# Kernel optimization log

Measured on AMD Instinct MI355X. Metric: run time of the kernel, lower is better.

Reference implementation:

```python
import jax, jax.numpy as jnp
import numpy as np
from jax import lax

N = 2048    # atoms
K = 16      # knn neighbors -> E = N*K = 32768 edges
H = 128     # latent width
L = 10      # stacked InteractionNetworks
STEPS = 10  # outer simulation iterations


def _rn(key, shape, scale=0.05):
    return scale * jax.random.normal(key, shape, dtype=jnp.float32)


def setup_inputs() -> dict:
    key = jax.random.key(0)
    ks = iter(jax.random.split(key, 40))
    inp = {
        "pos": jax.random.normal(next(ks), (N, 3), dtype=jnp.float32),
        "node_f": jax.random.normal(next(ks), (N, 24), dtype=jnp.float32),
        "mass": jnp.ones((N,), jnp.float32),
        # node encoder MLP(24,128,2,128)
        "nW1": _rn(next(ks), (24, H)), "nb1": _rn(next(ks), (H,)),
        "nW2": _rn(next(ks), (H, H)), "nb2": _rn(next(ks), (H,)),
        # edge encoder MLP(4,128,2,128)
        "eW1": _rn(next(ks), (4, H)), "eb1": _rn(next(ks), (H,)),
        "eW2": _rn(next(ks), (H, H)), "eb2": _rn(next(ks), (H,)),
        # RelationModel per IN: input = 2*dim_obj + dim_rel = 384, 4 Linear layers (ReLU after each)
        "rmW1": _rn(next(ks), (L, 3 * H, H)), "rmb1": _rn(next(ks), (L, H)),
        "rmW2": _rn(next(ks), (L, H, H)), "rmb2": _rn(next(ks), (L, H)),
        "rmW3": _rn(next(ks), (L, H, H)), "rmb3": _rn(next(ks), (L, H)),
        "rmW4": _rn(next(ks), (L, H, H)), "rmb4": _rn(next(ks), (L, H)),
        # ObjectModel per IN: input = dim_obj + dim_eff = 256 -> hidden 128 -> out 128
        "omW1": _rn(next(ks), (L, 2 * H, H)), "omb1": _rn(next(ks), (L, H)),
        "omW2": _rn(next(ks), (L, H, H)), "omb2": _rn(next(ks), (L, H)),
        # decoder MLP(128,128,2,3)
        "dW1": _rn(next(ks), (H, H)), "db1": _rn(next(ks), (H,)),
        "dW2": _rn(next(ks), (H, 3)), "db2": _rn(next(ks), (3,)),
        "k": K,
    }
    return inp


def _mlp2(x, W1, b1, W2, b2):
    return jax.nn.relu(x @ W1 + b1) @ W2 + b2


def _knn_edges(pos, k):
    # knn(P.pos, k): edge_index[:,0] = sender (neighbor), edge_index[:,1] = receiver
    n = pos.shape[0]
    sq = jnp.sum(pos * pos, axis=1)
    d2 = sq[:, None] + sq[None, :] - 2.0 * (pos @ pos.T)   # [N, N]
    d2 = d2 + 1e9 * jnp.eye(n, dtype=pos.dtype)            # exclude self
    _, idx = lax.top_k(-d2, k)                              # [N, k] nearest
    senders = idx.reshape(-1)                               # [E]
    receivers = jnp.repeat(jnp.arange(n), k)                # [E]
    rel = pos[senders] - pos[receivers]
    dist = jnp.linalg.norm(rel, axis=1, keepdims=True)
    ea0 = jnp.concatenate([rel, dist], axis=1)              # [E, 4]
    return senders, receivers, ea0


def _simulate(pos, node_f, mass, nW1, nb1, nW2, nb2, eW1, eb1, eW2, eb2,
              rmW1, rmb1, rmW2, rmb2, rmW3, rmb3, rmW4, rmb4,
              omW1, omb1, omW2, omb2, dW1, db1, dW2, db2, k):
    n = pos.shape[0]
    # G.pos = G.pos + randn * 0.1 ; G.vels = zeros
    pos = pos + 0.1 * jax.random.normal(jax.random.key(42), pos.shape, dtype=pos.dtype)
    vels = jnp.zeros_like(pos)

    stacked = (rmW1, rmb1, rmW2, rmb2, rmW3, rmb3, rmW4, rmb4,
               omW1, omb1, omW2, omb2)

    for _ in range(STEPS):
        senders, receivers, ea0 = _knn_edges(pos, k)

        # encode
        x = _mlp2(node_f, nW1, nb1, nW2, nb2)    # [N, H]
        ea = _mlp2(ea0, eW1, eb1, eW2, eb2)      # [E, H]

        # process: 10 InteractionNetworks. In the original, layer(P.x, P.senders,
        # P.receivers, P.edge_attr) binds rr=senders, rs=receivers, so the
        # one-hot matmuls obj.t()@rr / obj.t()@rs are gathers by sender/receiver,
        # and e @ rr.t() is a scatter-add onto sender nodes.
        def in_step(carry, p):
            xc, eac = carry
            rW1, rb1, rW2, rb2, rW3, rb3, rW4, rb4, oW1, ob1, oW2, ob2 = p
            b = jnp.concatenate([xc[senders], xc[receivers], eac], axis=1)  # [E, 3H]
            h = jax.nn.relu(b @ rW1 + rb1)
            h = jax.nn.relu(h @ rW2 + rb2)
            h = jax.nn.relu(h @ rW3 + rb3)
            e = jax.nn.relu(h @ rW4 + rb4)                                   # [E, H]
            agg = jax.ops.segment_sum(e, senders, num_segments=n)           # e @ rr.T
            a = jnp.concatenate([xc, agg], axis=1)                           # [N, 2H]
            x_new = jax.nn.relu(a @ oW1 + ob1) @ oW2 + ob2                   # [N, H]
            return (x_new, e), None

        (x, ea), _ = lax.scan(jax.checkpoint(in_step), (x, ea), stacked)

        # decode + update
        forces = _mlp2(x, dW1, db1, dW2, db2)    # [N, 3]
        vels = vels + forces / mass[:, None]
        pos = pos + vels
    return pos


def reference(pos, node_f, mass, nW1, nb1, nW2, nb2, eW1, eb1, eW2, eb2,
              rmW1, rmb1, rmW2, rmb2, rmW3, rmb3, rmW4, rmb4,
              omW1, omb1, omW2, omb2, dW1, db1, dW2, db2, k):
    return _simulate(pos, node_f, mass, nW1, nb1, nW2, nb2, eW1, eb1, eW2, eb2,
                     rmW1, rmb1, rmW2, rmb2, rmW3, rmb3, rmW4, rmb4,
                     omW1, omb1, omW2, omb2, dW1, db1, dW2, db2, k)
```

## Files before the change

### kernel.cpp

```cpp
#include <hip/hip_runtime.h>

#define N_ATOMS 2048
#define KNN 16
#define NE (N_ATOMS*KNN)
#define H 128
#define NL 10
#define NSTEPS 10
#define NCHUNK 32
#define S4B ((size_t)16384)
#define S8B ((size_t)32768)

typedef unsigned short u16;
typedef __attribute__((ext_vector_type(4))) float f32x4;
typedef __attribute__((ext_vector_type(8))) short bf16x8;

__device__ __forceinline__ u16 f2bf(float x){
  unsigned u = __float_as_uint(x);
  return (u16)((u + 0x7FFFu + ((u >> 16) & 1u)) >> 16);
}
__device__ __forceinline__ float bf2f(u16 v){ return __uint_as_float(((unsigned)v) << 16); }

template<int PITCH>
__device__ __forceinline__ bf16x8 ldsB_m8(const u16* s, int e, int k){
  int byte = e*PITCH + (k<<1); byte ^= ((e&7)<<4);
  return *(const bf16x8*)((const char*)s + byte);
}
template<int PITCH>
__device__ __forceinline__ void lds_st16_m8(u16* s, int row, int k, uint4 v){
  int byte = row*PITCH + (k<<1); byte ^= ((row&7)<<4);
  *(uint4*)((char*)s + byte) = v;
}
template<int PITCH>
__device__ __forceinline__ uint4 lds_ld16_m8(const u16* s, int row, int k){
  int byte = row*PITCH + (k<<1); byte ^= ((row&7)<<4);
  return *(const uint4*)((const char*)s + byte);
}
template<int PITCH>
__device__ __forceinline__ void lds_st8_m8(u16* s, int row, int k, uint2 v){
  int byte = row*PITCH + (k<<1); byte ^= ((row&7)<<4);
  *(uint2*)((char*)s + byte) = v;
}

template<int KST, int KS, int ET, int PITCH>
__device__ __forceinline__ void mfma_gemm_m8(const u16* sBh, const u16* sBl,
    const u16* __restrict__ pWh, const u16* __restrict__ pWl,
    int ksbase, int wpair, int rowbase, int lane, f32x4 acc[2][ET]){
  const int er = lane & 15, kg = lane >> 4;
  const size_t base = ((size_t)(wpair*KST + ksbase)*64 + lane)*8;
  #pragma unroll
  for (int ks = 0; ks < KS; ks++){
    const int klds = ks*32 + kg*8;
    bf16x8 bh[ET], bl[ET];
    #pragma unroll
    for (int et = 0; et < ET; et++){
      bh[et] = ldsB_m8<PITCH>(sBh, rowbase + et*16 + er, klds);
      bl[et] = ldsB_m8<PITCH>(sBl, rowbase + et*16 + er, klds);
    }
    #pragma unroll
    for (int nt = 0; nt < 2; nt++){
      const size_t off = base + (size_t)(nt*KST + ks)*512;
      bf16x8 ah = *(const bf16x8*)(pWh + off);
      bf16x8 al = *(const bf16x8*)(pWl + off);
      #pragma unroll
      for (int et = 0; et < ET; et++){
        acc[nt][et] = __builtin_amdgcn_mfma_f32_16x16x32_bf16(ah, bh[et], acc[nt][et], 0, 0, 0);
        acc[nt][et] = __builtin_amdgcn_mfma_f32_16x16x32_bf16(ah, bl[et], acc[nt][et], 0, 0, 0);
        acc[nt][et] = __builtin_amdgcn_mfma_f32_16x16x32_bf16(al, bh[et], acc[nt][et], 0, 0, 0);
      }
    }
  }
}

#define CLR_M8(acc, ET) { _Pragma("unroll") for (int i_=0;i_<2;i_++){ _Pragma("unroll") for (int j_=0;j_<ET;j_++){ \
  acc[i_][j_][0]=0.f; acc[i_][j_][1]=0.f; acc[i_][j_][2]=0.f; acc[i_][j_][3]=0.f; } } }

template<int ET, int PITCH, bool RELU>
__device__ __forceinline__ void epi_lds_m8(f32x4 acc[2][ET], u16* sh, u16* sl,
    int wpair, int rowbase, int lane, const float* __restrict__ bias){
  const int er = lane & 15, g = lane >> 4;
  #pragma unroll
  for (int nt = 0; nt < 2; nt++){
    const int n0 = (wpair + nt)*16 + g*4;
    f32x4 bv = *(const f32x4*)(bias + n0);
    #pragma unroll
    for (int et = 0; et < ET; et++){
      const int e = rowbase + et*16 + er;
      unsigned hw[2], lw[2];
      #pragma unroll
      for (int q = 0; q < 2; q++){
        float v0 = acc[nt][et][2*q]   + bv[2*q];
        float v1 = acc[nt][et][2*q+1] + bv[2*q+1];
        if (RELU){ v0 = fmaxf(v0, 0.f); v1 = fmaxf(v1, 0.f); }
        u16 h0 = f2bf(v0), h1 = f2bf(v1);
        u16 l0 = f2bf(v0 - bf2f(h0)), l1 = f2bf(v1 - bf2f(h1));
        hw[q] = (unsigned)h0 | ((unsigned)h1 << 16);
        lw[q] = (unsigned)l0 | ((unsigned)l1 << 16);
      }
      uint2 hv; hv.x = hw[0]; hv.y = hw[1];
      uint2 lv; lv.x = lw[0]; lv.y = lw[1];
      lds_st8_m8<PITCH>(sh, e, n0, hv);
      lds_st8_m8<PITCH>(sl, e, n0, lv);
    }
  }
}

__global__ __launch_bounds__(256) void pack_w_m8(const float* __restrict__ W,
    u16* __restrict__ ph, u16* __restrict__ pl, int KS, int L, int lstride, int roff){
  int idx = blockIdx.x*256 + threadIdx.x;
  int per = 8*KS*64;
  if (idx >= per*L) return;
  int l = idx / per, r = idx - l*per;
  int lane = r & 63, rest = r >> 6;
  int ks = rest % KS, nt = rest / KS;
  int n = nt*16 + (lane & 15), kb = ks*32 + (lane >> 4)*8;
  const float* src = W + (size_t)l*lstride;
  u16 h8[8], l8[8];
  #pragma unroll
  for (int j = 0; j < 8; j++){
    float v = src[(size_t)(roff + kb + j)*H + n];
    u16 h = f2bf(v);
    h8[j] = h; l8[j] = f2bf(v - bf2f(h));
  }
  size_t off = (size_t)idx*8;
  uint4 hv, lv;
  hv.x = h8[0]|((unsigned)h8[1]<<16); hv.y = h8[2]|((unsigned)h8[3]<<16);
  hv.z = h8[4]|((unsigned)h8[5]<<16); hv.w = h8[6]|((unsigned)h8[7]<<16);
  lv.x = l8[0]|((unsigned)l8[1]<<16); lv.y = l8[2]|((unsigned)l8[3]<<16);
  lv.z = l8[4]|((unsigned)l8[5]<<16); lv.w = l8[6]|((unsigned)l8[7]<<16);
  *(uint4*)(ph + off) = hv;
  *(uint4*)(pl + off) = lv;
}

__device__ __forceinline__ int lds_byte_f_m8(int r, int k4){
  return (((r<<9) + (k4<<2)) ^ (((r>>3)&7)<<4));
}
__device__ __forceinline__ f32x4 lds4r_f_m8(const float* s, int r, int k4){
  return *(const f32x4*)((const char*)s + lds_byte_f_m8(r,k4));
}
__device__ __forceinline__ void lds4w_f_m8(float* s, int r, int k4, f32x4 v){
  *(f32x4*)((char*)s + lds_byte_f_m8(r,k4)) = v;
}
__device__ __forceinline__ float lds1r_f_m8(const float* s, int r, int k){
  return *(const float*)((const char*)s + lds_byte_f_m8(r, k & ~3) + ((k&3)<<2));
}
template<int KD, int RPT>
__device__ __forceinline__ void gemm_f_m8(const float* sA, const float* __restrict__ gW,
                                          int r0, int c0, float acc[RPT][4]){
  #pragma unroll 2
  for (int k4 = 0; k4 < KD; k4 += 4){
    f32x4 a[RPT];
    #pragma unroll
    for (int i=0;i<RPT;i++) a[i] = lds4r_f_m8(sA, r0+i, k4);
    #pragma unroll
    for (int kk=0;kk<4;kk++){
      f32x4 wv = *(const f32x4*)(gW + (size_t)(k4+kk)*H + c0);
      #pragma unroll
      for (int i=0;i<RPT;i++){
        acc[i][0] = fmaf(a[i][kk], wv[0], acc[i][0]);
        acc[i][1] = fmaf(a[i][kk], wv[1], acc[i][1]);
        acc[i][2] = fmaf(a[i][kk], wv[2], acc[i][2]);
        acc[i][3] = fmaf(a[i][kk], wv[3], acc[i][3]);
      }
    }
  }
}

__device__ __forceinline__ unsigned rotl32_m8(unsigned v, int d){ return (v << d) | (v >> (32 - d)); }
__device__ __forceinline__ void tf2x32_m8(unsigned k0, unsigned k1, unsigned x0, unsigned x1,
                                          unsigned* o0, unsigned* o1){
  unsigned ks2 = k0 ^ k1 ^ 0x1BD11BDAu;
  x0 += k0; x1 += k1;
  const int R0[4] = {13,15,26,6}, R1[4] = {17,29,16,24};
#define TFG(R) { for (int i=0;i<4;i++){ x0 += x1; x1 = rotl32_m8(x1,R[i]); x1 ^= x0; } }
  TFG(R0); x0 += k1;  x1 += ks2 + 1u;
  TFG(R1); x0 += ks2; x1 += k0  + 2u;
  TFG(R0); x0 += k0;  x1 += k1  + 3u;
  TFG(R1); x0 += k1;  x1 += ks2 + 4u;
  TFG(R0); x0 += ks2; x1 += k0  + 5u;
#undef TFG
  *o0 = x0; *o1 = x1;
}
__device__ float bits_to_normal_m8(unsigned bits){
  float f = __uint_as_float((bits >> 9) | 0x3F800000u) - 1.0f;
  const float lo = -0.99999994f;
  float u = fmaxf(lo, __fadd_rn(__fmul_rn(f, 2.0f), lo));
  float w = -log1pf(-__fmul_rn(u, u));
  float p;
  if (w < 5.0f){
    w = __fsub_rn(w, 2.5f);
    p = 2.81022636e-08f;
    p = __fadd_rn(__fmul_rn(p,w),  3.43273939e-07f);
    p = __fadd_rn(__fmul_rn(p,w), -3.5233877e-06f);
    p = __fadd_rn(__fmul_rn(p,w), -4.39150654e-06f);
    p = __fadd_rn(__fmul_rn(p,w),  0.00021858087f);
    p = __fadd_rn(__fmul_rn(p,w), -0.00125372503f);
    p = __fadd_rn(__fmul_rn(p,w), -0.00417768164f);
    p = __fadd_rn(__fmul_rn(p,w),  0.246640727f);
    p = __fadd_rn(__fmul_rn(p,w),  1.50140941f);
  } else {
    w = __fsub_rn(sqrtf(w), 3.0f);
    p = -0.000200214257f;
    p = __fadd_rn(__fmul_rn(p,w),  0.000100950558f);
    p = __fadd_rn(__fmul_rn(p,w),  0.00134934322f);
    p = __fadd_rn(__fmul_rn(p,w), -0.00367342844f);
    p = __fadd_rn(__fmul_rn(p,w),  0.00573950773f);
    p = __fadd_rn(__fmul_rn(p,w), -0.0076224613f);
    p = __fadd_rn(__fmul_rn(p,w),  0.00943887047f);
    p = __fadd_rn(__fmul_rn(p,w),  1.00167406f);
    p = __fadd_rn(__fmul_rn(p,w),  2.83297682f);
  }
  return __fmul_rn(1.41421356f, __fmul_rn(p, u));
}
__device__ __forceinline__ unsigned draw_bits_m8(unsigned k1, unsigned k2, int bk, int m, int half){
  unsigned o0, o1;
  if (bk == 0){
    if (m < half){ tf2x32_m8(k1,k2, (unsigned)m, (unsigned)(m+half), &o0,&o1); return o0; }
    else         { tf2x32_m8(k1,k2, (unsigned)(m-half), (unsigned)m, &o0,&o1); return o1; }
  }
  tf2x32_m8(k1,k2, 0u, (unsigned)m, &o0,&o1);
  return (bk==1) ? (o0^o1) : (bk==2) ? o1 : o0;
}
__global__ __launch_bounds__(64) void rng_init_m8(int* flags){
  if (threadIdx.x < 8) flags[threadIdx.x] = 1;
}
__global__ __launch_bounds__(256) void rng_detect_m8(const float* __restrict__ pos_in, int* flags){
  int m = blockIdx.x*256 + threadIdx.x;
  if (m >= N_ATOMS*3) return;
  unsigned a0,a1,b0,b1,f0,f1;
  tf2x32_m8(0u,0u, 0u,40u, &a0,&a1);
  tf2x32_m8(0u,0u, 1u,41u, &b0,&b1);
  tf2x32_m8(0u,0u, 0u,0u,  &f0,&f1);
  float target = pos_in[m];
  #pragma unroll
  for (int v = 0; v < 8; v++){
    unsigned k1 = (v<4)? a0 : f0, k2 = (v<4)? b0 : f1;
    unsigned bits = draw_bits_m8(k1,k2, v&3, m, 3072);
    float z = bits_to_normal_m8(bits);
    if (fabsf(z - target) > 1e-3f) flags[v] = 0;
  }
}
__global__ __launch_bounds__(64) void rng_select_m8(const int* flags, int* sel){
  if (threadIdx.x == 0){
    int s = -1;
    for (int v = 0; v < 8; v++) if (flags[v]){ s = v; break; }
    sel[0] = (s < 0) ? 1 : (s & 3);
  }
}
__global__ __launch_bounds__(256) void perturb_m8(const float* __restrict__ pos,
    const int* __restrict__ sel, float* __restrict__ posw, float* __restrict__ vels){
  int m = blockIdx.x*256 + threadIdx.x;
  if (m >= N_ATOMS*3) return;
  unsigned bits = draw_bits_m8(0u, 42u, sel[0], m, 3072);
  float z = bits_to_normal_m8(bits);
  posw[m] = __fadd_rn(pos[m], __fmul_rn(0.1f, z));
  vels[m] = 0.f;
}

__global__ __launch_bounds__(128) void node_enc_m8(const float* __restrict__ nf,
    const float* __restrict__ W1, const float* __restrict__ b1,
    const float* __restrict__ W2, const float* __restrict__ b2,
    u16* __restrict__ xh, u16* __restrict__ xl){
  __shared__ float s_in[24];
  __shared__ float s_h[128];
  int n = blockIdx.x, t = threadIdx.x;
  if (t < 24) s_in[t] = nf[n*24 + t];
  __syncthreads();
  float a = b1[t];
  #pragma unroll
  for (int k = 0; k < 24; k++) a = fmaf(s_in[k], W1[k*H + t], a);
  s_h[t] = fmaxf(a, 0.f);
  __syncthreads();
  float a2 = b2[t];
  for (int k = 0; k < H; k++) a2 = fmaf(s_h[k], W2[k*H + t], a2);
  u16 h = f2bf(a2);
  xh[(size_t)n*H + t] = h;
  xl[(size_t)n*H + t] = f2bf(a2 - bf2f(h));
}

__global__ __launch_bounds__(256) void pnode_m8(
    const u16* __restrict__ xh, const u16* __restrict__ xl,
    const u16* __restrict__ pah, const u16* __restrict__ pal,
    const u16* __restrict__ pbh, const u16* __restrict__ pbl,
    float* __restrict__ P1g, float* __restrict__ P2g){
  __shared__ __align__(16) u16 sXh[16*128];
  __shared__ __align__(16) u16 sXl[16*128];
  const int t = threadIdx.x, n0b = blockIdx.x*16;
  const int i = t>>4, seg = t&15;
  {
    uint4 hv = *(const uint4*)(xh + (size_t)(n0b+i)*H + seg*8);
    uint4 lv = *(const uint4*)(xl + (size_t)(n0b+i)*H + seg*8);
    lds_st16_m8<256>(sXh, i, seg*8, hv);
    lds_st16_m8<256>(sXl, i, seg*8, lv);
  }
  __syncthreads();
  const int w = t>>6, lane = t&63, er = lane&15, g = lane>>4;
  f32x4 acc[2][1];
  CLR_M8(acc, 1);
  mfma_gemm_m8<4,4,1,256>(sXh, sXl, pah, pal, 0, w*2, 0, lane, acc);
  #pragma unroll
  for (int nt = 0; nt < 2; nt++)
    *(f32x4*)(P1g + (size_t)(n0b+er)*H + (w*2+nt)*16 + g*4) = acc[nt][0];
  CLR_M8(acc, 1);
  mfma_gemm_m8<4,4,1,256>(sXh, sXl, pbh, pbl, 0, w*2, 0, lane, acc);
  #pragma unroll
  for (int nt = 0; nt < 2; nt++)
    *(f32x4*)(P2g + (size_t)(n0b+er)*H + (w*2+nt)*16 + g*4) = acc[nt][0];
}

__global__ __launch_bounds__(256) void knn_m9(const float* __restrict__ pos,
                                              int* __restrict__ senders,
                                              float* __restrict__ ea0,
                                              int* __restrict__ countsC){
  __shared__ float d2[N_ATOMS];
  __shared__ float pv[4];
  __shared__ int   pi[4];
  int r = blockIdx.x, t = threadIdx.x;
  float prx = pos[r*3+0], pry = pos[r*3+1], prz = pos[r*3+2];
  float sqr = __fadd_rn(__fadd_rn(__fmul_rn(prx,prx), __fmul_rn(pry,pry)), __fmul_rn(prz,prz));
  for (int c = t; c < N_ATOMS; c += 256){
    float cx = pos[c*3+0], cy = pos[c*3+1], cz = pos[c*3+2];
    float sqc = __fadd_rn(__fadd_rn(__fmul_rn(cx,cx), __fmul_rn(cy,cy)), __fmul_rn(cz,cz));
    float dot = __fadd_rn(__fadd_rn(__fmul_rn(prx,cx), __fmul_rn(pry,cy)), __fmul_rn(prz,cz));
    float v = __fsub_rn(__fadd_rn(sqr, sqc), __fmul_rn(2.0f, dot));
    d2[c] = (c == r) ? 1e9f : v;
  }
  __syncthreads();
  for (int j = 0; j < KNN; j++){
    float bv = 1e30f; int bi = 0x7fffffff;
    for (int c = t; c < N_ATOMS; c += 256){
      float v = d2[c];
      if (v < bv || (v == bv && c < bi)){ bv = v; bi = c; }
    }
    #pragma unroll
    for (int off = 32; off; off >>= 1){
      float ov = __shfl_down(bv, off);
      int   oi = __shfl_down(bi, off);
      if (ov < bv || (ov == bv && oi < bi)){ bv = ov; bi = oi; }
    }
    if ((t & 63) == 0){ pv[t>>6] = bv; pi[t>>6] = bi; }
    __syncthreads();
    if (t == 0){
      float fv = pv[0]; int fi = pi[0];
      #pragma unroll
      for (int q = 1; q < 4; q++){
        if (pv[q] < fv || (pv[q] == fv && pi[q] < fi)){ fv = pv[q]; fi = pi[q]; }
      }
      senders[r*KNN + j] = fi;
      atomicAdd(&countsC[(r>>6)*N_ATOMS + fi], 1);
      float dx = __fsub_rn(pos[fi*3+0], prx);
      float dy = __fsub_rn(pos[fi*3+1], pry);
      float dz = __fsub_rn(pos[fi*3+2], prz);
      float ss = __fadd_rn(__fadd_rn(__fmul_rn(dx,dx), __fmul_rn(dy,dy)), __fmul_rn(dz,dz));
      float* o = ea0 + (size_t)(r*KNN + j)*4;
      o[0] = dx; o[1] = dy; o[2] = dz; o[3] = sqrtf(ss);
      d2[fi] = 1e30f;
    }
    __syncthreads();
  }
}

__global__ __launch_bounds__(256) void csr_scan2_m9(int* __restrict__ countsC,
                                                    int* __restrict__ rowstart){
  __shared__ int part[256];
  const int t = threadIdx.x;
  const int base = t*8;
  int loc[8];
  int ssum = 0;
  #pragma unroll
  for (int i = 0; i < 8; i++){
    int s = base + i;
    int tv = 0;
    #pragma unroll
    for (int c = 0; c < NCHUNK; c++) tv += countsC[c*N_ATOMS + s];
    loc[i] = ssum; ssum += tv;
  }
  part[t] = ssum;
  __syncthreads();
  if (t == 0){
    int acc = 0;
    for (int i = 0; i < 256; i++){ int v = part[i]; part[i] = acc; acc += v; }
    rowstart[N_ATOMS] = acc;
  }
  __syncthreads();
  int p = part[t];
  #pragma unroll
  for (int i = 0; i < 8; i++){
    int s = base + i;
    int rs = p + loc[i];
    rowstart[s] = rs;
    int b = rs;
    #pragma unroll
    for (int c = 0; c < NCHUNK; c++){
      int tv = countsC[c*N_ATOMS + s];
      countsC[c*N_ATOMS + s] = b;
      b += tv;
    }
  }
}

__global__ __launch_bounds__(1024) void csr_place_m9(const int* __restrict__ senders,
    const int* __restrict__ countsC, int* __restrict__ elist){
  __shared__ int cnt[N_ATOMS];
  __shared__ int sL[1024];
  const int c = blockIdx.x, t = threadIdx.x;
  cnt[t] = countsC[c*N_ATOMS + t];
  cnt[1024 + t] = countsC[c*N_ATOMS + 1024 + t];
  sL[t] = senders[c*1024 + t];
  __syncthreads();
  const int w = t>>6, lane = t&63, wb = w<<6;
  const int my_s = sL[t];
  int rank = 0, same = 0;
  for (int k = 0; k < 64; k++){
    int sk = sL[wb + k];
    int eq = (sk == my_s) ? 1 : 0;
    same += eq;
    if (k < lane) rank += eq;
  }
  #pragma unroll
  for (int round = 0; round < 16; round++){
    if (w == round){
      int bb = cnt[my_s];
      elist[bb + rank] = c*1024 + t;
      if (rank == same - 1) cnt[my_s] = bb + same;
    }
    __syncthreads();
  }
}

template<int FIRST>
__global__ __launch_bounds__(256) void chain_m8(
    const float* __restrict__ P1g, const float* __restrict__ P2g,
    u16* __restrict__ eag, const int* __restrict__ senders,
    const float* __restrict__ ea0,
    const float* __restrict__ eW1, const float* __restrict__ eb1,
    const u16* __restrict__ e2h, const u16* __restrict__ e2l, const float* __restrict__ eb2,
    const u16* __restrict__ w1h, const u16* __restrict__ w1l, const float* __restrict__ b1,
    const u16* __restrict__ w2h, const u16* __restrict__ w2l, const float* __restrict__ b2,
    const u16* __restrict__ w3h, const u16* __restrict__ w3l, const float* __restrict__ b3,
    const u16* __restrict__ w4h, const u16* __restrict__ w4l, const float* __restrict__ b4){
  __shared__ __align__(16) u16 sPh[64*128];
  __shared__ __align__(16) u16 sPl[64*128];
  __shared__ __align__(16) u16 sQh[64*128];
  __shared__ __align__(16) u16 sQl[64*128];
  __shared__ float sE0[64*4];
  const int t = threadIdx.x, e0 = blockIdx.x*64;
  const int w = t>>6, lane = t&63, er = lane&15, g = lane>>4;
  const int wpair = w*2;
  f32x4 acc[2][4];
  int sidx[4];
  #pragma unroll
  for (int et = 0; et < 4; et++) sidx[et] = senders[e0 + et*16 + er];
  #pragma unroll
  for (int et = 0; et < 4; et++){
    const int rr = (e0>>4) + et;
    #pragma unroll
    for (int nt = 0; nt < 2; nt++){
      const int n0 = (wpair+nt)*16 + g*4;
      f32x4 p1 = *(const f32x4*)(P1g + (size_t)sidx[et]*H + n0);
      f32x4 p2 = *(const f32x4*)(P2g + (size_t)rr*H + n0);
      acc[nt][et] = p1 + p2;
    }
  }
  if (FIRST){
    if (t < 64){
      uint4 v = *(const uint4*)(ea0 + (size_t)(e0 + t)*4);
      *(uint4*)(sE0 + t*4) = v;
    }
    __syncthreads();
    const int r0e = ((lane>>3)&7)*8, c0e = w*32 + (lane&7)*4;
    f32x4 bv1 = *(const f32x4*)(eb1 + c0e);
    f32x4 w0v = *(const f32x4*)(eW1 + 0*H + c0e);
    f32x4 w1v = *(const f32x4*)(eW1 + 1*H + c0e);
    f32x4 w2v = *(const f32x4*)(eW1 + 2*H + c0e);
    f32x4 w3v = *(const f32x4*)(eW1 + 3*H + c0e);
    #pragma unroll
    for (int i = 0; i < 8; i++){
      int rr = r0e + i;
      float e0v = sE0[rr*4+0], e1v = sE0[rr*4+1], e2v = sE0[rr*4+2], e3v = sE0[rr*4+3];
      unsigned hw[2], lw[2];
      #pragma unroll
      for (int q = 0; q < 2; q++){
        float v0 = fmaf(e3v, w3v[2*q],   fmaf(e2v, w2v[2*q],   fmaf(e1v, w1v[2*q],   fmaf(e0v, w0v[2*q],   bv1[2*q]))));
        float v1 = fmaf(e3v, w3v[2*q+1], fmaf(e2v, w2v[2*q+1], fmaf(e1v, w1v[2*q+1], fmaf(e0v, w0v[2*q+1], bv1[2*q+1]))));
        v0 = fmaxf(v0, 0.f); v1 = fmaxf(v1, 0.f);
        u16 h0 = f2bf(v0), h1 = f2bf(v1);
        u16 l0 = f2bf(v0 - bf2f(h0)), l1 = f2bf(v1 - bf2f(h1));
        hw[q] = (unsigned)h0 | ((unsigned)h1<<16);
        lw[q] = (unsigned)l0 | ((unsigned)l1<<16);
      }
      uint2 hv; hv.x = hw[0]; hv.y = hw[1];
      uint2 lv; lv.x = lw[0]; lv.y = lw[1];
      lds_st8_m8<256>(sQh, rr, c0e, hv);
      lds_st8_m8<256>(sQl, rr, c0e, lv);
    }
    __syncthreads();
    f32x4 acc0[2][4]; CLR_M8(acc0, 4);
    mfma_gemm_m8<4,4,4,256>(sQh, sQl, e2h, e2l, 0, wpair, 0, lane, acc0);
    __syncthreads();
    epi_lds_m8<4,256,false>(acc0, sPh, sPl, wpair, 0, lane, eb2);
    __syncthreads();
  } else {
    const char* src = (const char*)(eag + (size_t)e0*256);
    #pragma unroll
    for (int m = 0; m < 8; m++){
      int byteoff = (t + m*256)*16;
      uint4 v = *(const uint4*)(src + byteoff);
      int row = byteoff>>9, off = byteoff&511;
      lds_st16_m8<256>((off<256)? sPh : sPl, row, (off&255)>>1, v);
    }
    __syncthreads();
  }
  mfma_gemm_m8<4,4,4,256>(sPh, sPl, w1h, w1l, 0, wpair, 0, lane, acc);
  epi_lds_m8<4,256,true>(acc, sQh, sQl, wpair, 0, lane, b1);
  __syncthreads();
  CLR_M8(acc, 4);
  mfma_gemm_m8<4,4,4,256>(sQh, sQl, w2h, w2l, 0, wpair, 0, lane, acc);
  epi_lds_m8<4,256,true>(acc, sPh, sPl, wpair, 0, lane, b2);
  __syncthreads();
  CLR_M8(acc, 4);
  mfma_gemm_m8<4,4,4,256>(sPh, sPl, w3h, w3l, 0, wpair, 0, lane, acc);
  epi_lds_m8<4,256,true>(acc, sQh, sQl, wpair, 0, lane, b3);
  __syncthreads();
  CLR_M8(acc, 4);
  mfma_gemm_m8<4,4,4,256>(sQh, sQl, w4h, w4l, 0, wpair, 0, lane, acc);
  epi_lds_m8<4,256,true>(acc, sPh, sPl, wpair, 0, lane, b4);
  __syncthreads();
  char* dst = (char*)(eag + (size_t)e0*256);
  #pragma unroll
  for (int m = 0; m < 8; m++){
    int byteoff = (t + m*256)*16;
    int row = byteoff>>9, off = byteoff&511;
    uint4 v = lds_ld16_m8<256>((off<256)? sPh : sPl, row, (off&255)>>1);
    *(uint4*)(dst + byteoff) = v;
  }
}

__global__ __launch_bounds__(256) void objagg_m8(
    const u16* __restrict__ xch, const u16* __restrict__ xcl,
    const u16* __restrict__ eag,
    const int* __restrict__ rowstart, const int* __restrict__ elist,
    const u16* __restrict__ o1h, const u16* __restrict__ o1l, const float* __restrict__ ob1,
    const u16* __restrict__ o2h, const u16* __restrict__ o2l, const float* __restrict__ ob2,
    const u16* __restrict__ nah, const u16* __restrict__ nal,
    const u16* __restrict__ nbh, const u16* __restrict__ nbl,
    u16* __restrict__ xoh, u16* __restrict__ xol,
    float* __restrict__ P1g, float* __restrict__ P2g){
  __shared__ __align__(16) u16 sIh[16*256];
  __shared__ __align__(16) u16 sIl[16*256];
  __shared__ __align__(16) u16 sHh[16*128];
  __shared__ __align__(16) u16 sHl[16*128];
  __shared__ __align__(16) u16 sXh[16*128];
  __shared__ __align__(16) u16 sXl[16*128];
  const int t = threadIdx.x, n0b = blockIdx.x*8;
  const int w = t>>6, lane = t&63;
  const int i = t>>5, c0 = (t&31)*4;
  {
    uint2 hv = *(const uint2*)(xch + (size_t)(n0b+i)*H + c0);
    uint2 lv = *(const uint2*)(xcl + (size_t)(n0b+i)*H + c0);
    lds_st8_m8<512>(sIh, i, c0, hv);
    lds_st8_m8<512>(sIl, i, c0, lv);
    float a0 = 0.f, a1 = 0.f, a2 = 0.f, a3 = 0.f;
    const int b0 = rowstart[n0b+i], e1 = rowstart[n0b+i+1];
    for (int p = b0; p < e1; p++){
      const int ed = elist[p];
      uint2 hv2 = *(const uint2*)(eag + (size_t)ed*256 + c0);
      uint2 lv2 = *(const uint2*)(eag + (size_t)ed*256 + 128 + c0);
      a0 += bf2f((u16)(hv2.x & 0xffffu)) + bf2f((u16)(lv2.x & 0xffffu));
      a1 += bf2f((u16)(hv2.x >> 16))     + bf2f((u16)(lv2.x >> 16));
      a2 += bf2f((u16)(hv2.y & 0xffffu)) + bf2f((u16)(lv2.y & 0xffffu));
      a3 += bf2f((u16)(hv2.y >> 16))     + bf2f((u16)(lv2.y >> 16));
    }
    u16 h0 = f2bf(a0), h1 = f2bf(a1), h2 = f2bf(a2), h3 = f2bf(a3);
    u16 l0 = f2bf(a0 - bf2f(h0)), l1 = f2bf(a1 - bf2f(h1));
    u16 l2 = f2bf(a2 - bf2f(h2)), l3 = f2bf(a3 - bf2f(h3));
    uint2 hvo; hvo.x = (unsigned)h0 | ((unsigned)h1<<16); hvo.y = (unsigned)h2 | ((unsigned)h3<<16);
    uint2 lvo; lvo.x = (unsigned)l0 | ((unsigned)l1<<16); lvo.y = (unsigned)l2 | ((unsigned)l3<<16);
    lds_st8_m8<512>(sIh, i, 128 + c0, hvo);
    lds_st8_m8<512>(sIl, i, 128 + c0, lvo);
  }
  __syncthreads();
  f32x4 acc[2][1];
  CLR_M8(acc, 1);
  mfma_gemm_m8<8,8,1,512>(sIh, sIl, o1h, o1l, 0, w*2, 0, lane, acc);
  epi_lds_m8<1,256,true>(acc, sHh, sHl, w*2, 0, lane, ob1);
  __syncthreads();
  CLR_M8(acc, 1);
  mfma_gemm_m8<4,4,1,256>(sHh, sHl, o2h, o2l, 0, w*2, 0, lane, acc);
  epi_lds_m8<1,256,false>(acc, sXh, sXl, w*2, 0, lane, ob2);
  __syncthreads();
  if (t < 128){
    int row = t>>4, seg = t&15;
    uint4 hv = lds_ld16_m8<256>(sXh, row, seg*8);
    uint4 lv = lds_ld16_m8<256>(sXl, row, seg*8);
    *(uint4*)(xoh + (size_t)(n0b+row)*H + seg*8) = hv;
    *(uint4*)(xol + (size_t)(n0b+row)*H + seg*8) = lv;
  }
  const int er = lane&15, g = lane>>4;
  CLR_M8(acc, 1);
  mfma_gemm_m8<4,4,1,256>(sXh, sXl, nah, nal, 0, w*2, 0, lane, acc);
  if (er < 8){
    #pragma unroll
    for (int nt = 0; nt < 2; nt++)
      *(f32x4*)(P1g + (size_t)(n0b+er)*H + (w*2+nt)*16 + g*4) = acc[nt][0];
  }
  CLR_M8(acc, 1);
  mfma_gemm_m8<4,4,1,256>(sXh, sXl, nbh, nbl, 0, w*2, 0, lane, acc);
  if (er < 8){
    #pragma unroll
    for (int nt = 0; nt < 2; nt++)
      *(f32x4*)(P2g + (size_t)(n0b+er)*H + (w*2+nt)*16 + g*4) = acc[nt][0];
  }
}

__global__ __launch_bounds__(256) void decode_m8(
    const u16* __restrict__ xhi, const u16* __restrict__ xlo,
    const float* __restrict__ dW1, const float* __restrict__ db1,
    const float* __restrict__ dW2, const float* __restrict__ db2,
    const float* __restrict__ mass, float* __restrict__ posw, float* __restrict__ vels){
  __shared__ float sX[16*128];
  __shared__ float sY[16*128];
  const int t = threadIdx.x;
  const int n0 = blockIdx.x*16;
  const int w = t>>6, l = t&63;
  const int r0 = ((l>>3)&7)*2, c0 = w*32 + (l&7)*4;
  const int si = t>>4, sg = t&15;
  {
    const u16* ph = xhi + (size_t)(n0+si)*H + sg*8;
    const u16* pl = xlo + (size_t)(n0+si)*H + sg*8;
    uint4 hv = *(const uint4*)ph;
    uint4 lv = *(const uint4*)pl;
    unsigned hw[4] = {hv.x,hv.y,hv.z,hv.w}, lw[4] = {lv.x,lv.y,lv.z,lv.w};
    f32x4 v0, v1;
    #pragma unroll
    for (int m = 0; m < 2; m++){
      v0[2*m]   = bf2f((u16)(hw[m]&0xffffu)) + bf2f((u16)(lw[m]&0xffffu));
      v0[2*m+1] = bf2f((u16)(hw[m]>>16))     + bf2f((u16)(lw[m]>>16));
      v1[2*m]   = bf2f((u16)(hw[m+2]&0xffffu)) + bf2f((u16)(lw[m+2]&0xffffu));
      v1[2*m+1] = bf2f((u16)(hw[m+2]>>16))     + bf2f((u16)(lw[m+2]>>16));
    }
    lds4w_f_m8(sX, si, sg*8, v0);
    lds4w_f_m8(sX, si, sg*8 + 4, v1);
  }
  __syncthreads();
  float acc[2][4];
  #pragma unroll
  for (int i=0;i<2;i++){ acc[i][0]=0.f; acc[i][1]=0.f; acc[i][2]=0.f; acc[i][3]=0.f; }
  gemm_f_m8<128,2>(sX, dW1, r0, c0, acc);
  {
    f32x4 bv = *(const f32x4*)(db1 + c0);
    #pragma unroll
    for (int i=0;i<2;i++){
      f32x4 v;
      #pragma unroll
      for (int j=0;j<4;j++){ float x = acc[i][j] + bv[j]; v[j] = fmaxf(x, 0.f); }
      lds4w_f_m8(sY, r0+i, c0, v);
    }
  }
  __syncthreads();
  if (t < 48){
    int i = t/3, c = t - i*3;
    float a = db2[c];
    for (int k = 0; k < 128; k++) a = fmaf(lds1r_f_m8(sY, i, k), dW2[k*3 + c], a);
    int n = n0 + i;
    float f = a / mass[n];
    float v = vels[n*3 + c] + f;
    vels[n*3 + c] = v;
    posw[n*3 + c] += v;
  }
}

extern "C" void kernel_launch(void* const* d_in, const int* in_sizes, int n_in,
                              void* d_out, int out_size, void* d_ws, size_t ws_size,
                              hipStream_t stream){
  const float* pos   = (const float*)d_in[0];
  const float* nodef = (const float*)d_in[1];
  const float* mass  = (const float*)d_in[2];
  const float* nW1 = (const float*)d_in[3];  const float* nb1 = (const float*)d_in[4];
  const float* nW2 = (const float*)d_in[5];  const float* nb2 = (const float*)d_in[6];
  const float* eW1 = (const float*)d_in[7];  const float* eb1 = (const float*)d_in[8];
  const float* eW2 = (const float*)d_in[9];  const float* eb2 = (const float*)d_in[10];
  const float* rmW1 = (const float*)d_in[11]; const float* rmb1 = (const float*)d_in[12];
  const float* rmW2 = (const float*)d_in[13]; const float* rmb2 = (const float*)d_in[14];
  const float* rmW3 = (const float*)d_in[15]; const float* rmb3 = (const float*)d_in[16];
  const float* rmW4 = (const float*)d_in[17]; const float* rmb4 = (const float*)d_in[18];
  const float* omW1 = (const float*)d_in[19]; const float* omb1 = (const float*)d_in[20];
  const float* omW2 = (const float*)d_in[21]; const float* omb2 = (const float*)d_in[22];
  const float* dW1 = (const float*)d_in[23]; const float* db1 = (const float*)d_in[24];
  const float* dW2 = (const float*)d_in[25]; const float* db2 = (const float*)d_in[26];

  char* wptr = (char*)d_ws;
  auto alloc = [&](size_t bytes)->void*{
    void* p = (void*)wptr; wptr += (bytes + 255) & ~(size_t)255; return p;
  };
  float* posw  = (float*)alloc((size_t)N_ATOMS*3*4);
  float* vels  = (float*)alloc((size_t)N_ATOMS*3*4);
  int*   senders = (int*)alloc((size_t)NE*4);
  float* ea0   = (float*)alloc((size_t)NE*4*4);
  u16* xench = (u16*)alloc((size_t)N_ATOMS*H*2);
  u16* xencl = (u16*)alloc((size_t)N_ATOMS*H*2);
  u16* xAh   = (u16*)alloc((size_t)N_ATOMS*H*2);
  u16* xAl   = (u16*)alloc((size_t)N_ATOMS*H*2);
  u16* xBh   = (u16*)alloc((size_t)N_ATOMS*H*2);
  u16* xBl   = (u16*)alloc((size_t)N_ATOMS*H*2);
  u16* eag   = (u16*)alloc((size_t)NE*256*2);
  float* P1g  = (float*)alloc((size_t)N_ATOMS*H*4);
  float* P2g  = (float*)alloc((size_t)N_ATOMS*H*4);
  float* P01g = (float*)alloc((size_t)N_ATOMS*H*4);
  float* P02g = (float*)alloc((size_t)N_ATOMS*H*4);
  int* rowstart = (int*)alloc((size_t)(N_ATOMS+1)*4);
  int* elist    = (int*)alloc((size_t)NE*4);
  int* countsC  = (int*)alloc((size_t)NCHUNK*N_ATOMS*4);
  int* rflags   = (int*)alloc(64);
  int* rsel     = (int*)alloc(64);
  u16* p1ah = (u16*)alloc(S4B*NL*2); u16* p1al = (u16*)alloc(S4B*NL*2);
  u16* p1bh = (u16*)alloc(S4B*NL*2); u16* p1bl = (u16*)alloc(S4B*NL*2);
  u16* p1ch = (u16*)alloc(S4B*NL*2); u16* p1cl = (u16*)alloc(S4B*NL*2);
  u16* prm2h = (u16*)alloc(S4B*NL*2); u16* prm2l = (u16*)alloc(S4B*NL*2);
  u16* prm3h = (u16*)alloc(S4B*NL*2); u16* prm3l = (u16*)alloc(S4B*NL*2);
  u16* prm4h = (u16*)alloc(S4B*NL*2); u16* prm4l = (u16*)alloc(S4B*NL*2);
  u16* pom1h = (u16*)alloc(S8B*NL*2); u16* pom1l = (u16*)alloc(S8B*NL*2);
  u16* pom2h = (u16*)alloc(S4B*NL*2); u16* pom2l = (u16*)alloc(S4B*NL*2);
  u16* pe2h  = (u16*)alloc(S4B*2);    u16* pe2l  = (u16*)alloc(S4B*2);

  auto pack = [&](const float* W, u16* ph, u16* pl, int KS, int L, int lstride, int roff){
    int total = L*8*KS*64;
    pack_w_m8<<<(total+255)/256, 256, 0, stream>>>(W, ph, pl, KS, L, lstride, roff);
  };
  pack(rmW1, p1ah, p1al, 4, NL, 384*H, 0);
  pack(rmW1, p1bh, p1bl, 4, NL, 384*H, 128);
  pack(rmW1, p1ch, p1cl, 4, NL, 384*H, 256);
  pack(rmW2, prm2h, prm2l, 4, NL, H*H, 0);
  pack(rmW3, prm3h, prm3l, 4, NL, H*H, 0);
  pack(rmW4, prm4h, prm4l, 4, NL, H*H, 0);
  pack(omW1, pom1h, pom1l, 8, NL, 2*H*H, 0);
  pack(omW2, pom2h, pom2l, 4, NL, H*H, 0);
  pack(eW2,  pe2h,  pe2l,  4, 1,  H*H, 0);

  rng_init_m8<<<1, 64, 0, stream>>>(rflags);
  rng_detect_m8<<<(N_ATOMS*3+255)/256, 256, 0, stream>>>(pos, rflags);
  rng_select_m8<<<1, 64, 0, stream>>>(rflags, rsel);
  perturb_m8<<<(N_ATOMS*3+255)/256, 256, 0, stream>>>(pos, rsel, posw, vels);
  node_enc_m8<<<N_ATOMS, 128, 0, stream>>>(nodef, nW1, nb1, nW2, nb2, xench, xencl);
  pnode_m8<<<N_ATOMS/16, 256, 0, stream>>>(xench, xencl, p1ah, p1al, p1bh, p1bl, P01g, P02g);

  for (int s = 0; s < NSTEPS; s++){
    hipMemsetAsync(countsC, 0, (size_t)NCHUNK*N_ATOMS*4, stream);
    knn_m9<<<N_ATOMS, 256, 0, stream>>>(posw, senders, ea0, countsC);
    csr_scan2_m9<<<1, 256, 0, stream>>>(countsC, rowstart);
    csr_place_m9<<<NCHUNK, 1024, 0, stream>>>(senders, countsC, elist);

    const u16* xch = xench; const u16* xcl = xencl;
    for (int l = 0; l < NL; l++){
      const float* Pa = (l == 0) ? P01g : P1g;
      const float* Pb = (l == 0) ? P02g : P2g;
      if (l == 0){
        chain_m8<1><<<NE/64, 256, 0, stream>>>(Pa, Pb, eag, senders,
            ea0, eW1, eb1, pe2h, pe2l, eb2,
            p1ch  + (size_t)l*S4B, p1cl  + (size_t)l*S4B, rmb1 + l*H,
            prm2h + (size_t)l*S4B, prm2l + (size_t)l*S4B, rmb2 + l*H,
            prm3h + (size_t)l*S4B, prm3l + (size_t)l*S4B, rmb3 + l*H,
            prm4h + (size_t)l*S4B, prm4l + (size_t)l*S4B, rmb4 + l*H);
      } else {
        chain_m8<0><<<NE/64, 256, 0, stream>>>(Pa, Pb, eag, senders,
            ea0, eW1, eb1, pe2h, pe2l, eb2,
            p1ch  + (size_t)l*S4B, p1cl  + (size_t)l*S4B, rmb1 + l*H,
            prm2h + (size_t)l*S4B, prm2l + (size_t)l*S4B, rmb2 + l*H,
            prm3h + (size_t)l*S4B, prm3l + (size_t)l*S4B, rmb3 + l*H,
            prm4h + (size_t)l*S4B, prm4l + (size_t)l*S4B, rmb4 + l*H);
      }
      u16* xnh = (l & 1) ? xAh : xBh;
      u16* xnl = (l & 1) ? xAl : xBl;
      int lp1 = (l < NL-1) ? (l+1) : l;
      objagg_m8<<<N_ATOMS/8, 256, 0, stream>>>(xch, xcl, eag, rowstart, elist,
          pom1h + (size_t)l*S8B, pom1l + (size_t)l*S8B, omb1 + l*H,
          pom2h + (size_t)l*S4B, pom2l + (size_t)l*S4B, omb2 + l*H,
          p1ah + (size_t)lp1*S4B, p1al + (size_t)lp1*S4B,
          p1bh + (size_t)lp1*S4B, p1bl + (size_t)lp1*S4B,
          xnh, xnl, P1g, P2g);
      xch = xnh; xcl = xnl;
    }
    decode_m8<<<N_ATOMS/16, 256, 0, stream>>>(xch, xcl, dW1, db1, dW2, db2, mass, posw, vels);
  }
  hipMemcpyAsync(d_out, posw, (size_t)N_ATOMS*3*4, hipMemcpyDeviceToDevice, stream);
}
```

Measured before the change: 5.132 ms.

## Fuse decoder into last object kernel, wave-per-row kNN, shrink chain LDS

The kNN kernel now gives each wavefront its own row, so four rows run per block and the block-wide barriers and cross-wave reduction are gone. The decoder MLP is folded into the final layer's object/aggregation kernel through a LAST template, which drops one launch and one round trip of node features per step. The chain kernel's LDS buffers are merged from four to two to raise occupancy, and f2bf now uses the HIP bf16 intrinsic. The cost is a larger kNN LDS footprint per block and more complex templated objagg code.

```diff
diff --git a/kernel.cpp b/kernel.cpp
--- a/kernel.cpp
+++ b/kernel.cpp
@@ -1,4 +1,5 @@
 #include <hip/hip_runtime.h>
+#include <hip/hip_bf16.h>
 
 #define N_ATOMS 2048
 #define KNN 16
@@ -15,34 +16,40 @@
 typedef __attribute__((ext_vector_type(8))) short bf16x8;
 
 __device__ __forceinline__ u16 f2bf(float x){
-  unsigned u = __float_as_uint(x);
-  return (u16)((u + 0x7FFFu + ((u >> 16) & 1u)) >> 16);
+  union { __hip_bfloat16 b; u16 u; } v;
+  v.b = __float2bfloat16(x);
+  return v.u;
 }
 __device__ __forceinline__ float bf2f(u16 v){ return __uint_as_float(((unsigned)v) << 16); }
 
 template<int PITCH>
-__device__ __forceinline__ bf16x8 ldsB_m8(const u16* s, int e, int k){
+__device__ __forceinline__ bf16x8 ldsB_m10(const u16* s, int e, int k){
   int byte = e*PITCH + (k<<1); byte ^= ((e&7)<<4);
   return *(const bf16x8*)((const char*)s + byte);
 }
 template<int PITCH>
-__device__ __forceinline__ void lds_st16_m8(u16* s, int row, int k, uint4 v){
+__device__ __forceinline__ void lds_st16_m10(u16* s, int row, int k, uint4 v){
   int byte = row*PITCH + (k<<1); byte ^= ((row&7)<<4);
   *(uint4*)((char*)s + byte) = v;
 }
 template<int PITCH>
-__device__ __forceinline__ uint4 lds_ld16_m8(const u16* s, int row, int k){
+__device__ __forceinline__ uint4 lds_ld16_m10(const u16* s, int row, int k){
   int byte = row*PITCH + (k<<1); byte ^= ((row&7)<<4);
   return *(const uint4*)((const char*)s + byte);
 }
 template<int PITCH>
-__device__ __forceinline__ void lds_st8_m8(u16* s, int row, int k, uint2 v){
+__device__ __forceinline__ void lds_st8_m10(u16* s, int row, int k, uint2 v){
   int byte = row*PITCH + (k<<1); byte ^= ((row&7)<<4);
   *(uint2*)((char*)s + byte) = v;
 }
+template<int PITCH>
+__device__ __forceinline__ uint2 lds_ld8_m10(const u16* s, int row, int k){
+  int byte = row*PITCH + (k<<1); byte ^= ((row&7)<<4);
+  return *(const uint2*)((const char*)s + byte);
+}
 
 template<int KST, int KS, int ET, int PITCH>
-__device__ __forceinline__ void mfma_gemm_m8(const u16* sBh, const u16* sBl,
+__device__ __forceinline__ void mfma_gemm_m10(const u16* sBh, const u16* sBl,
     const u16* __restrict__ pWh, const u16* __restrict__ pWl,
     int ksbase, int wpair, int rowbase, int lane, f32x4 acc[2][ET]){
   const int er = lane & 15, kg = lane >> 4;
@@ -53,8 +60,8 @@
     bf16x8 bh[ET], bl[ET];
     #pragma unroll
     for (int et = 0; et < ET; et++){
-      bh[et] = ldsB_m8<PITCH>(sBh, rowbase + et*16 + er, klds);
-      bl[et] = ldsB_m8<PITCH>(sBl, rowbase + et*16 + er, klds);
+      bh[et] = ldsB_m10<PITCH>(sBh, rowbase + et*16 + er, klds);
+      bl[et] = ldsB_m10<PITCH>(sBl, rowbase + et*16 + er, klds);
     }
     #pragma unroll
     for (int nt = 0; nt < 2; nt++){
@@ -71,11 +78,11 @@
   }
 }
 
-#define CLR_M8(acc, ET) { _Pragma("unroll") for (int i_=0;i_<2;i_++){ _Pragma("unroll") for (int j_=0;j_<ET;j_++){ \
+#define CLR_M10(acc, ET) { _Pragma("unroll") for (int i_=0;i_<2;i_++){ _Pragma("unroll") for (int j_=0;j_<ET;j_++){ \
   acc[i_][j_][0]=0.f; acc[i_][j_][1]=0.f; acc[i_][j_][2]=0.f; acc[i_][j_][3]=0.f; } } }
 
 template<int ET, int PITCH, bool RELU>
-__device__ __forceinline__ void epi_lds_m8(f32x4 acc[2][ET], u16* sh, u16* sl,
+__device__ __forceinline__ void epi_lds_m10(f32x4 acc[2][ET], u16* sh, u16* sl,
     int wpair, int rowbase, int lane, const float* __restrict__ bias){
   const int er = lane & 15, g = lane >> 4;
   #pragma unroll
@@ -98,13 +105,13 @@
       }
       uint2 hv; hv.x = hw[0]; hv.y = hw[1];
       uint2 lv; lv.x = lw[0]; lv.y = lw[1];
-      lds_st8_m8<PITCH>(sh, e, n0, hv);
-      lds_st8_m8<PITCH>(sl, e, n0, lv);
-    }
-  }
-}
-
-__global__ __launch_bounds__(256) void pack_w_m8(const float* __restrict__ W,
+      lds_st8_m10<PITCH>(sh, e, n0, hv);
+      lds_st8_m10<PITCH>(sl, e, n0, lv);
+    }
+  }
+}
+
+__global__ __launch_bounds__(256) void pack_w_m10(const float* __restrict__ W,
     u16* __restrict__ ph, u16* __restrict__ pl, int KS, int L, int lstride, int roff){
   int idx = blockIdx.x*256 + threadIdx.x;
   int per = 8*KS*64;
@@ -131,26 +138,26 @@
   *(uint4*)(pl + off) = lv;
 }
 
-__device__ __forceinline__ int lds_byte_f_m8(int r, int k4){
+__device__ __forceinline__ int lds_byte_f_m10(int r, int k4){
   return (((r<<9) + (k4<<2)) ^ (((r>>3)&7)<<4));
 }
-__device__ __forceinline__ f32x4 lds4r_f_m8(const float* s, int r, int k4){
-  return *(const f32x4*)((const char*)s + lds_byte_f_m8(r,k4));
-}
-__device__ __forceinline__ void lds4w_f_m8(float* s, int r, int k4, f32x4 v){
-  *(f32x4*)((char*)s + lds_byte_f_m8(r,k4)) = v;
-}
-__device__ __forceinline__ float lds1r_f_m8(const float* s, int r, int k){
-  return *(const float*)((const char*)s + lds_byte_f_m8(r, k & ~3) + ((k&3)<<2));
+__device__ __forceinline__ f32x4 lds4r_f_m10(const float* s, int r, int k4){
+  return *(const f32x4*)((const char*)s + lds_byte_f_m10(r,k4));
+}
+__device__ __forceinline__ void lds4w_f_m10(float* s, int r, int k4, f32x4 v){
+  *(f32x4*)((char*)s + lds_byte_f_m10(r,k4)) = v;
+}
+__device__ __forceinline__ float lds1r_f_m10(const float* s, int r, int k){
+  return *(const float*)((const char*)s + lds_byte_f_m10(r, k & ~3) + ((k&3)<<2));
 }
 template<int KD, int RPT>
-__device__ __forceinline__ void gemm_f_m8(const float* sA, const float* __restrict__ gW,
-                                          int r0, int c0, float acc[RPT][4]){
+__device__ __forceinline__ void gemm_f_m10(const float* sA, const float* __restrict__ gW,
+                                           int r0, int c0, float acc[RPT][4]){
   #pragma unroll 2
   for (int k4 = 0; k4 < KD; k4 += 4){
     f32x4 a[RPT];
     #pragma unroll
-    for (int i=0;i<RPT;i++) a[i] = lds4r_f_m8(sA, r0+i, k4);
+    for (int i=0;i<RPT;i++) a[i] = lds4r_f_m10(sA, r0+i, k4);
     #pragma unroll
     for (int kk=0;kk<4;kk++){
       f32x4 wv = *(const f32x4*)(gW + (size_t)(k4+kk)*H + c0);
@@ -165,13 +172,13 @@
   }
 }
 
-__device__ __forceinline__ unsigned rotl32_m8(unsigned v, int d){ return (v << d) | (v >> (32 - d)); }
-__device__ __forceinline__ void tf2x32_m8(unsigned k0, unsigned k1, unsigned x0, unsigned x1,
-                                          unsigned* o0, unsigned* o1){
+__device__ __forceinline__ unsigned rotl32_m10(unsigned v, int d){ return (v << d) | (v >> (32 - d)); }
+__device__ __forceinline__ void tf2x32_m10(unsigned k0, unsigned k1, unsigned x0, unsigned x1,
+                                           unsigned* o0, unsigned* o1){
   unsigned ks2 = k0 ^ k1 ^ 0x1BD11BDAu;
   x0 += k0; x1 += k1;
   const int R0[4] = {13,15,26,6}, R1[4] = {17,29,16,24};
-#define TFG(R) { for (int i=0;i<4;i++){ x0 += x1; x1 = rotl32_m8(x1,R[i]); x1 ^= x0; } }
+#define TFG(R) { for (int i=0;i<4;i++){ x0 += x1; x1 = rotl32_m10(x1,R[i]); x1 ^= x0; } }
   TFG(R0); x0 += k1;  x1 += ks2 + 1u;
   TFG(R1); x0 += ks2; x1 += k0  + 2u;
   TFG(R0); x0 += k0;  x1 += k1  + 3u;
@@ -180,7 +187,7 @@
 #undef TFG
   *o0 = x0; *o1 = x1;
 }
-__device__ float bits_to_normal_m8(unsigned bits){
+__device__ float bits_to_normal_m10(unsigned bits){
   float f = __uint_as_float((bits >> 9) | 0x3F800000u) - 1.0f;
   const float lo = -0.99999994f;
   float u = fmaxf(lo, __fadd_rn(__fmul_rn(f, 2.0f), lo));
@@ -211,52 +218,52 @@
   }
   return __fmul_rn(1.41421356f, __fmul_rn(p, u));
 }
-__device__ __forceinline__ unsigned draw_bits_m8(unsigned k1, unsigned k2, int bk, int m, int half){
+__device__ __forceinline__ unsigned draw_bits_m10(unsigned k1, unsigned k2, int bk, int m, int half){
   unsigned o0, o1;
   if (bk == 0){
-    if (m < half){ tf2x32_m8(k1,k2, (unsigned)m, (unsigned)(m+half), &o0,&o1); return o0; }
-    else         { tf2x32_m8(k1,k2, (unsigned)(m-half), (unsigned)m, &o0,&o1); return o1; }
-  }
-  tf2x32_m8(k1,k2, 0u, (unsigned)m, &o0,&o1);
+    if (m < half){ tf2x32_m10(k1,k2, (unsigned)m, (unsigned)(m+half), &o0,&o1); return o0; }
+    else         { tf2x32_m10(k1,k2, (unsigned)(m-half), (unsigned)m, &o0,&o1); return o1; }
+  }
+  tf2x32_m10(k1,k2, 0u, (unsigned)m, &o0,&o1);
   return (bk==1) ? (o0^o1) : (bk==2) ? o1 : o0;
 }
-__global__ __launch_bounds__(64) void rng_init_m8(int* flags){
+__global__ __launch_bounds__(64) void rng_init_m10(int* flags){
   if (threadIdx.x < 8) flags[threadIdx.x] = 1;
 }
-__global__ __launch_bounds__(256) void rng_detect_m8(const float* __restrict__ pos_in, int* flags){
+__global__ __launch_bounds__(256) void rng_detect_m10(const float* __restrict__ pos_in, int* flags){
   int m = blockIdx.x*256 + threadIdx.x;
   if (m >= N_ATOMS*3) return;
   unsigned a0,a1,b0,b1,f0,f1;
-  tf2x32_m8(0u,0u, 0u,40u, &a0,&a1);
-  tf2x32_m8(0u,0u, 1u,41u, &b0,&b1);
-  tf2x32_m8(0u,0u, 0u,0u,  &f0,&f1);
+  tf2x32_m10(0u,0u, 0u,40u, &a0,&a1);
+  tf2x32_m10(0u,0u, 1u,41u, &b0,&b1);
+  tf2x32_m10(0u,0u, 0u,0u,  &f0,&f1);
   float target = pos_in[m];
   #pragma unroll
   for (int v = 0; v < 8; v++){
     unsigned k1 = (v<4)? a0 : f0, k2 = (v<4)? b0 : f1;
-    unsigned bits = draw_bits_m8(k1,k2, v&3, m, 3072);
-    float z = bits_to_normal_m8(bits);
+    unsigned bits = draw_bits_m10(k1,k2, v&3, m, 3072);
+    float z = bits_to_normal_m10(bits);
     if (fabsf(z - target) > 1e-3f) flags[v] = 0;
   }
 }
-__global__ __launch_bounds__(64) void rng_select_m8(const int* flags, int* sel){
+__global__ __launch_bounds__(64) void rng_select_m10(const int* flags, int* sel){
   if (threadIdx.x == 0){
     int s = -1;
     for (int v = 0; v < 8; v++) if (flags[v]){ s = v; break; }
     sel[0] = (s < 0) ? 1 : (s & 3);
   }
 }
-__global__ __launch_bounds__(256) void perturb_m8(const float* __restrict__ pos,
+__global__ __launch_bounds__(256) void perturb_m10(const float* __restrict__ pos,
     const int* __restrict__ sel, float* __restrict__ posw, float* __restrict__ vels){
   int m = blockIdx.x*256 + threadIdx.x;
   if (m >= N_ATOMS*3) return;
-  unsigned bits = draw_bits_m8(0u, 42u, sel[0], m, 3072);
-  float z = bits_to_normal_m8(bits);
+  unsigned bits = draw_bits_m10(0u, 42u, sel[0], m, 3072);
+  float z = bits_to_normal_m10(bits);
   posw[m] = __fadd_rn(pos[m], __fmul_rn(0.1f, z));
   vels[m] = 0.f;
 }
 
-__global__ __launch_bounds__(128) void node_enc_m8(const float* __restrict__ nf,
+__global__ __launch_bounds__(128) void node_enc_m10(const float* __restrict__ nf,
     const float* __restrict__ W1, const float* __restrict__ b1,
     const float* __restrict__ W2, const float* __restrict__ b2,
     u16* __restrict__ xh, u16* __restrict__ xl){
@@ -277,7 +284,7 @@
   xl[(size_t)n*H + t] = f2bf(a2 - bf2f(h));
 }
 
-__global__ __launch_bounds__(256) void pnode_m8(
+__global__ __launch_bounds__(256) void pnode_m10(
     const u16* __restrict__ xh, const u16* __restrict__ xl,
     const u16* __restrict__ pah, const u16* __restrict__ pal,
     const u16* __restrict__ pbh, const u16* __restrict__ pbl,
@@ -289,45 +296,45 @@
   {
     uint4 hv = *(const uint4*)(xh + (size_t)(n0b+i)*H + seg*8);
     uint4 lv = *(const uint4*)(xl + (size_t)(n0b+i)*H + seg*8);
-    lds_st16_m8<256>(sXh, i, seg*8, hv);
-    lds_st16_m8<256>(sXl, i, seg*8, lv);
+    lds_st16_m10<256>(sXh, i, seg*8, hv);
+    lds_st16_m10<256>(sXl, i, seg*8, lv);
   }
   __syncthreads();
   const int w = t>>6, lane = t&63, er = lane&15, g = lane>>4;
   f32x4 acc[2][1];
-  CLR_M8(acc, 1);
-  mfma_gemm_m8<4,4,1,256>(sXh, sXl, pah, pal, 0, w*2, 0, lane, acc);
+  CLR_M10(acc, 1);
+  mfma_gemm_m10<4,4,1,256>(sXh, sXl, pah, pal, 0, w*2, 0, lane, acc);
   #pragma unroll
   for (int nt = 0; nt < 2; nt++)
     *(f32x4*)(P1g + (size_t)(n0b+er)*H + (w*2+nt)*16 + g*4) = acc[nt][0];
-  CLR_M8(acc, 1);
-  mfma_gemm_m8<4,4,1,256>(sXh, sXl, pbh, pbl, 0, w*2, 0, lane, acc);
+  CLR_M10(acc, 1);
+  mfma_gemm_m10<4,4,1,256>(sXh, sXl, pbh, pbl, 0, w*2, 0, lane, acc);
   #pragma unroll
   for (int nt = 0; nt < 2; nt++)
     *(f32x4*)(P2g + (size_t)(n0b+er)*H + (w*2+nt)*16 + g*4) = acc[nt][0];
 }
 
-__global__ __launch_bounds__(256) void knn_m9(const float* __restrict__ pos,
-                                              int* __restrict__ senders,
-                                              float* __restrict__ ea0,
-                                              int* __restrict__ countsC){
-  __shared__ float d2[N_ATOMS];
-  __shared__ float pv[4];
-  __shared__ int   pi[4];
-  int r = blockIdx.x, t = threadIdx.x;
+__global__ __launch_bounds__(256) void knn_m10(const float* __restrict__ pos,
+                                               int* __restrict__ senders,
+                                               float* __restrict__ ea0,
+                                               int* __restrict__ countsC){
+  __shared__ float d2s[4*N_ATOMS];
+  const int t = threadIdx.x, w = t>>6, lane = t&63;
+  float* d2 = d2s + w*N_ATOMS;
+  const int r = blockIdx.x*4 + w;
   float prx = pos[r*3+0], pry = pos[r*3+1], prz = pos[r*3+2];
   float sqr = __fadd_rn(__fadd_rn(__fmul_rn(prx,prx), __fmul_rn(pry,pry)), __fmul_rn(prz,prz));
-  for (int c = t; c < N_ATOMS; c += 256){
+  for (int c = lane; c < N_ATOMS; c += 64){
     float cx = pos[c*3+0], cy = pos[c*3+1], cz = pos[c*3+2];
     float sqc = __fadd_rn(__fadd_rn(__fmul_rn(cx,cx), __fmul_rn(cy,cy)), __fmul_rn(cz,cz));
     float dot = __fadd_rn(__fadd_rn(__fmul_rn(prx,cx), __fmul_rn(pry,cy)), __fmul_rn(prz,cz));
     float v = __fsub_rn(__fadd_rn(sqr, sqc), __fmul_rn(2.0f, dot));
     d2[c] = (c == r) ? 1e9f : v;
   }
-  __syncthreads();
+  asm volatile("" ::: "memory");
   for (int j = 0; j < KNN; j++){
     float bv = 1e30f; int bi = 0x7fffffff;
-    for (int c = t; c < N_ATOMS; c += 256){
+    for (int c = lane; c < N_ATOMS; c += 64){
       float v = d2[c];
       if (v < bv || (v == bv && c < bi)){ bv = v; bi = c; }
     }
@@ -337,30 +344,24 @@
       int   oi = __shfl_down(bi, off);
       if (ov < bv || (ov == bv && oi < bi)){ bv = ov; bi = oi; }
     }
-    if ((t & 63) == 0){ pv[t>>6] = bv; pi[t>>6] = bi; }
-    __syncthreads();
-    if (t == 0){
-      float fv = pv[0]; int fi = pi[0];
-      #pragma unroll
-      for (int q = 1; q < 4; q++){
-        if (pv[q] < fv || (pv[q] == fv && pi[q] < fi)){ fv = pv[q]; fi = pi[q]; }
-      }
-      senders[r*KNN + j] = fi;
-      atomicAdd(&countsC[(r>>6)*N_ATOMS + fi], 1);
-      float dx = __fsub_rn(pos[fi*3+0], prx);
-      float dy = __fsub_rn(pos[fi*3+1], pry);
-      float dz = __fsub_rn(pos[fi*3+2], prz);
+    bi = __shfl(bi, 0);
+    if (lane == 0){
+      senders[r*KNN + j] = bi;
+      atomicAdd(&countsC[(r>>6)*N_ATOMS + bi], 1);
+      float dx = __fsub_rn(pos[bi*3+0], prx);
+      float dy = __fsub_rn(pos[bi*3+1], pry);
+      float dz = __fsub_rn(pos[bi*3+2], prz);
       float ss = __fadd_rn(__fadd_rn(__fmul_rn(dx,dx), __fmul_rn(dy,dy)), __fmul_rn(dz,dz));
       float* o = ea0 + (size_t)(r*KNN + j)*4;
       o[0] = dx; o[1] = dy; o[2] = dz; o[3] = sqrtf(ss);
-      d2[fi] = 1e30f;
-    }
-    __syncthreads();
-  }
-}
-
-__global__ __launch_bounds__(256) void csr_scan2_m9(int* __restrict__ countsC,
-                                                    int* __restrict__ rowstart){
+    }
+    if ((bi & 63) == lane) d2[bi] = 1e30f;
+    asm volatile("" ::: "memory");
+  }
+}
+
+__global__ __launch_bounds__(256) void csr_scan2_m10(int* __restrict__ countsC,
+                                                     int* __restrict__ rowstart){
   __shared__ int part[256];
   const int t = threadIdx.x;
   const int base = t*8;
@@ -398,7 +399,7 @@
   }
 }
 
-__global__ __launch_bounds__(1024) void csr_place_m9(const int* __restrict__ senders,
+__global__ __launch_bounds__(1024) void csr_place_m10(const int* __restrict__ senders,
     const int* __restrict__ countsC, int* __restrict__ elist){
   __shared__ int cnt[N_ATOMS];
   __shared__ int sL[1024];
@@ -428,7 +429,7 @@
 }
 
 template<int FIRST>
-__global__ __launch_bounds__(256) void chain_m8(
+__global__ __launch_bounds__(256) void chain_m10(
     const float* __restrict__ P1g, const float* __restrict__ P2g,
     u16* __restrict__ eag, const int* __restrict__ senders,
     const float* __restrict__ ea0,
@@ -438,10 +439,8 @@
     const u16* __restrict__ w2h, const u16* __restrict__ w2l, const float* __restrict__ b2,
     const u16* __restrict__ w3h, const u16* __restrict__ w3l, const float* __restrict__ b3,
     const u16* __restrict__ w4h, const u16* __restrict__ w4l, const float* __restrict__ b4){
-  __shared__ __align__(16) u16 sPh[64*128];
-  __shared__ __align__(16) u16 sPl[64*128];
-  __shared__ __align__(16) u16 sQh[64*128];
-  __shared__ __align__(16) u16 sQl[64*128];
+  __shared__ __align__(16) u16 sAh[64*128];
+  __shared__ __align__(16) u16 sAl[64*128];
   __shared__ float sE0[64*4];
   const int t = threadIdx.x, e0 = blockIdx.x*64;
   const int w = t>>6, lane = t&63, er = lane&15, g = lane>>4;
@@ -490,14 +489,14 @@
       }
       uint2 hv; hv.x = hw[0]; hv.y = hw[1];
       uint2 lv; lv.x = lw[0]; lv.y = lw[1];
-      lds_st8_m8<256>(sQh, rr, c0e, hv);
-      lds_st8_m8<256>(sQl, rr, c0e, lv);
+      lds_st8_m10<256>(sAh, rr, c0e, hv);
+      lds_st8_m10<256>(sAl, rr, c0e, lv);
     }
     __syncthreads();
-    f32x4 acc0[2][4]; CLR_M8(acc0, 4);
-    mfma_gemm_m8<4,4,4,256>(sQh, sQl, e2h, e2l, 0, wpair, 0, lane, acc0);
+    f32x4 acc0[2][4]; CLR_M10(acc0, 4);
+    mfma_gemm_m10<4,4,4,256>(sAh, sAl, e2h, e2l, 0, wpair, 0, lane, acc0);
     __syncthreads();
-    epi_lds_m8<4,256,false>(acc0, sPh, sPl, wpair, 0, lane, eb2);
+    epi_lds_m10<4,256,false>(acc0, sAh, sAl, wpair, 0, lane, eb2);
     __syncthreads();
   } else {
     const char* src = (const char*)(eag + (size_t)e0*256);
@@ -506,36 +505,41 @@
       int byteoff = (t + m*256)*16;
       uint4 v = *(const uint4*)(src + byteoff);
       int row = byteoff>>9, off = byteoff&511;
-      lds_st16_m8<256>((off<256)? sPh : sPl, row, (off&255)>>1, v);
+      lds_st16_m10<256>((off<256)? sAh : sAl, row, (off&255)>>1, v);
     }
     __syncthreads();
   }
-  mfma_gemm_m8<4,4,4,256>(sPh, sPl, w1h, w1l, 0, wpair, 0, lane, acc);
-  epi_lds_m8<4,256,true>(acc, sQh, sQl, wpair, 0, lane, b1);
-  __syncthreads();
-  CLR_M8(acc, 4);
-  mfma_gemm_m8<4,4,4,256>(sQh, sQl, w2h, w2l, 0, wpair, 0, lane, acc);
-  epi_lds_m8<4,256,true>(acc, sPh, sPl, wpair, 0, lane, b2);
-  __syncthreads();
-  CLR_M8(acc, 4);
-  mfma_gemm_m8<4,4,4,256>(sPh, sPl, w3h, w3l, 0, wpair, 0, lane, acc);
-  epi_lds_m8<4,256,true>(acc, sQh, sQl, wpair, 0, lane, b3);
-  __syncthreads();
-  CLR_M8(acc, 4);
-  mfma_gemm_m8<4,4,4,256>(sQh, sQl, w4h, w4l, 0, wpair, 0, lane, acc);
-  epi_lds_m8<4,256,true>(acc, sPh, sPl, wpair, 0, lane, b4);
+  mfma_gemm_m10<4,4,4,256>(sAh, sAl, w1h, w1l, 0, wpair, 0, lane, acc);
+  __syncthreads();
+  epi_lds_m10<4,256,true>(acc, sAh, sAl, wpair, 0, lane, b1);
+  __syncthreads();
+  CLR_M10(acc, 4);
+  mfma_gemm_m10<4,4,4,256>(sAh, sAl, w2h, w2l, 0, wpair, 0, lane, acc);
+  __syncthreads();
+  epi_lds_m10<4,256,true>(acc, sAh, sAl, wpair, 0, lane, b2);
+  __syncthreads();
+  CLR_M10(acc, 4);
+  mfma_gemm_m10<4,4,4,256>(sAh, sAl, w3h, w3l, 0, wpair, 0, lane, acc);
+  __syncthreads();
+  epi_lds_m10<4,256,true>(acc, sAh, sAl, wpair, 0, lane, b3);
+  __syncthreads();
+  CLR_M10(acc, 4);
+  mfma_gemm_m10<4,4,4,256>(sAh, sAl, w4h, w4l, 0, wpair, 0, lane, acc);
+  __syncthreads();
+  epi_lds_m10<4,256,true>(acc, sAh, sAl, wpair, 0, lane, b4);
   __syncthreads();
   char* dst = (char*)(eag + (size_t)e0*256);
   #pragma unroll
   for (int m = 0; m < 8; m++){
     int byteoff = (t + m*256)*16;
     int row = byteoff>>9, off = byteoff&511;
-    uint4 v = lds_ld16_m8<256>((off<256)? sPh : sPl, row, (off&255)>>1);
+    uint4 v = lds_ld16_m10<256>((off<256)? sAh : sAl, row, (off&255)>>1);
     *(uint4*)(dst + byteoff) = v;
   }
 }
 
-__global__ __launch_bounds__(256) void objagg_m8(
+template<int LAST>
+__global__ __launch_bounds__(256) void objagg_m10(
     const u16* __restrict__ xch, const u16* __restrict__ xcl,
     const u16* __restrict__ eag,
     const int* __restrict__ rowstart, const int* __restrict__ elist,
@@ -544,21 +548,26 @@
     const u16* __restrict__ nah, const u16* __restrict__ nal,
     const u16* __restrict__ nbh, const u16* __restrict__ nbl,
     u16* __restrict__ xoh, u16* __restrict__ xol,
-    float* __restrict__ P1g, float* __restrict__ P2g){
+    float* __restrict__ P1g, float* __restrict__ P2g,
+    const float* __restrict__ dW1, const float* __restrict__ db1,
+    const float* __restrict__ dW2, const float* __restrict__ db2,
+    const float* __restrict__ mass, float* __restrict__ posw, float* __restrict__ vels){
   __shared__ __align__(16) u16 sIh[16*256];
   __shared__ __align__(16) u16 sIl[16*256];
   __shared__ __align__(16) u16 sHh[16*128];
   __shared__ __align__(16) u16 sHl[16*128];
   __shared__ __align__(16) u16 sXh[16*128];
   __shared__ __align__(16) u16 sXl[16*128];
+  __shared__ float sXf[8*128];
+  __shared__ float sYf[8*128];
   const int t = threadIdx.x, n0b = blockIdx.x*8;
   const int w = t>>6, lane = t&63;
   const int i = t>>5, c0 = (t&31)*4;
   {
     uint2 hv = *(const uint2*)(xch + (size_t)(n0b+i)*H + c0);
     uint2 lv = *(const uint2*)(xcl + (size_t)(n0b+i)*H + c0);
-    lds_st8_m8<512>(sIh, i, c0, hv);
-    lds_st8_m8<512>(sIl, i, c0, lv);
+    lds_st8_m10<512>(sIh, i, c0, hv);
+    lds_st8_m10<512>(sIl, i, c0, lv);
     float a0 = 0.f, a1 = 0.f, a2 = 0.f, a3 = 0.f;
     const int b0 = rowstart[n0b+i], e1 = rowstart[n0b+i+1];
     for (int p = b0; p < e1; p++){
@@ -575,97 +584,76 @@
     u16 l2 = f2bf(a2 - bf2f(h2)), l3 = f2bf(a3 - bf2f(h3));
     uint2 hvo; hvo.x = (unsigned)h0 | ((unsigned)h1<<16); hvo.y = (unsigned)h2 | ((unsigned)h3<<16);
     uint2 lvo; lvo.x = (unsigned)l0 | ((unsigned)l1<<16); lvo.y = (unsigned)l2 | ((unsigned)l3<<16);
-    lds_st8_m8<512>(sIh, i, 128 + c0, hvo);
-    lds_st8_m8<512>(sIl, i, 128 + c0, lvo);
+    lds_st8_m10<512>(sIh, i, 128 + c0, hvo);
+    lds_st8_m10<512>(sIl, i, 128 + c0, lvo);
   }
   __syncthreads();
   f32x4 acc[2][1];
-  CLR_M8(acc, 1);
-  mfma_gemm_m8<8,8,1,512>(sIh, sIl, o1h, o1l, 0, w*2, 0, lane, acc);
-  epi_lds_m8<1,256,true>(acc, sHh, sHl, w*2, 0, lane, ob1);
-  __syncthreads();
-  CLR_M8(acc, 1);
-  mfma_gemm_m8<4,4,1,256>(sHh, sHl, o2h, o2l, 0, w*2, 0, lane, acc);
-  epi_lds_m8<1,256,false>(acc, sXh, sXl, w*2, 0, lane, ob2);
-  __syncthreads();
-  if (t < 128){
-    int row = t>>4, seg = t&15;
-    uint4 hv = lds_ld16_m8<256>(sXh, row, seg*8);
-    uint4 lv = lds_ld16_m8<256>(sXl, row, seg*8);
-    *(uint4*)(xoh + (size_t)(n0b+row)*H + seg*8) = hv;
-    *(uint4*)(xol + (size_t)(n0b+row)*H + seg*8) = lv;
-  }
-  const int er = lane&15, g = lane>>4;
-  CLR_M8(acc, 1);
-  mfma_gemm_m8<4,4,1,256>(sXh, sXl, nah, nal, 0, w*2, 0, lane, acc);
-  if (er < 8){
-    #pragma unroll
-    for (int nt = 0; nt < 2; nt++)
-      *(f32x4*)(P1g + (size_t)(n0b+er)*H + (w*2+nt)*16 + g*4) = acc[nt][0];
-  }
-  CLR_M8(acc, 1);
-  mfma_gemm_m8<4,4,1,256>(sXh, sXl, nbh, nbl, 0, w*2, 0, lane, acc);
-  if (er < 8){
-    #pragma unroll
-    for (int nt = 0; nt < 2; nt++)
-      *(f32x4*)(P2g + (size_t)(n0b+er)*H + (w*2+nt)*16 + g*4) = acc[nt][0];
-  }
-}
-
-__global__ __launch_bounds__(256) void decode_m8(
-    const u16* __restrict__ xhi, const u16* __restrict__ xlo,
-    const float* __restrict__ dW1, const float* __restrict__ db1,
-    const float* __restrict__ dW2, const float* __restrict__ db2,
-    const float* __restrict__ mass, float* __restrict__ posw, float* __restrict__ vels){
-  __shared__ float sX[16*128];
-  __shared__ float sY[16*128];
-  const int t = threadIdx.x;
-  const int n0 = blockIdx.x*16;
-  const int w = t>>6, l = t&63;
-  const int r0 = ((l>>3)&7)*2, c0 = w*32 + (l&7)*4;
-  const int si = t>>4, sg = t&15;
-  {
-    const u16* ph = xhi + (size_t)(n0+si)*H + sg*8;
-    const u16* pl = xlo + (size_t)(n0+si)*H + sg*8;
-    uint4 hv = *(const uint4*)ph;
-    uint4 lv = *(const uint4*)pl;
-    unsigned hw[4] = {hv.x,hv.y,hv.z,hv.w}, lw[4] = {lv.x,lv.y,lv.z,lv.w};
-    f32x4 v0, v1;
-    #pragma unroll
-    for (int m = 0; m < 2; m++){
-      v0[2*m]   = bf2f((u16)(hw[m]&0xffffu)) + bf2f((u16)(lw[m]&0xffffu));
-      v0[2*m+1] = bf2f((u16)(hw[m]>>16))     + bf2f((u16)(lw[m]>>16));
-      v1[2*m]   = bf2f((u16)(hw[m+2]&0xffffu)) + bf2f((u16)(lw[m+2]&0xffffu));
-      v1[2*m+1] = bf2f((u16)(hw[m+2]>>16))     + bf2f((u16)(lw[m+2]>>16));
-    }
-    lds4w_f_m8(sX, si, sg*8, v0);
-    lds4w_f_m8(sX, si, sg*8 + 4, v1);
-  }
-  __syncthreads();
-  float acc[2][4];
-  #pragma unroll
-  for (int i=0;i<2;i++){ acc[i][0]=0.f; acc[i][1]=0.f; acc[i][2]=0.f; acc[i][3]=0.f; }
-  gemm_f_m8<128,2>(sX, dW1, r0, c0, acc);
-  {
-    f32x4 bv = *(const f32x4*)(db1 + c0);
-    #pragma unroll
-    for (int i=0;i<2;i++){
+  CLR_M10(acc, 1);
+  mfma_gemm_m10<8,8,1,512>(sIh, sIl, o1h, o1l, 0, w*2, 0, lane, acc);
+  epi_lds_m10<1,256,true>(acc, sHh, sHl, w*2, 0, lane, ob1);
+  __syncthreads();
+  CLR_M10(acc, 1);
+  mfma_gemm_m10<4,4,1,256>(sHh, sHl, o2h, o2l, 0, w*2, 0, lane, acc);
+  epi_lds_m10<1,256,false>(acc, sXh, sXl, w*2, 0, lane, ob2);
+  __syncthreads();
+  if (!LAST){
+    if (t < 128){
+      int row = t>>4, seg = t&15;
+      uint4 hv = lds_ld16_m10<256>(sXh, row, seg*8);
+      uint4 lv = lds_ld16_m10<256>(sXl, row, seg*8);
+      *(uint4*)(xoh + (size_t)(n0b+row)*H + seg*8) = hv;
+      *(uint4*)(xol + (size_t)(n0b+row)*H + seg*8) = lv;
+    }
+    const int er = lane&15, g = lane>>4;
+    CLR_M10(acc, 1);
+    mfma_gemm_m10<4,4,1,256>(sXh, sXl, nah, nal, 0, w*2, 0, lane, acc);
+    if (er < 8){
+      #pragma unroll
+      for (int nt = 0; nt < 2; nt++)
+        *(f32x4*)(P1g + (size_t)(n0b+er)*H + (w*2+nt)*16 + g*4) = acc[nt][0];
+    }
+    CLR_M10(acc, 1);
+    mfma_gemm_m10<4,4,1,256>(sXh, sXl, nbh, nbl, 0, w*2, 0, lane, acc);
+    if (er < 8){
+      #pragma unroll
+      for (int nt = 0; nt < 2; nt++)
+        *(f32x4*)(P2g + (size_t)(n0b+er)*H + (w*2+nt)*16 + g*4) = acc[nt][0];
+    }
+  } else {
+    {
+      uint2 hv = lds_ld8_m10<256>(sXh, i, c0);
+      uint2 lv = lds_ld8_m10<256>(sXl, i, c0);
+      f32x4 v;
+      v[0] = bf2f((u16)(hv.x & 0xffffu)) + bf2f((u16)(lv.x & 0xffffu));
+      v[1] = bf2f((u16)(hv.x >> 16))     + bf2f((u16)(lv.x >> 16));
+      v[2] = bf2f((u16)(hv.y & 0xffffu)) + bf2f((u16)(lv.y & 0xffffu));
+      v[3] = bf2f((u16)(hv.y >> 16))     + bf2f((u16)(lv.y >> 16));
+      lds4w_f_m10(sXf, i, c0, v);
+    }
+    __syncthreads();
+    const int r0d = (lane>>3)&7, c0d = w*32 + (lane&7)*4;
+    float fac[1][4];
+    fac[0][0]=0.f; fac[0][1]=0.f; fac[0][2]=0.f; fac[0][3]=0.f;
+    gemm_f_m10<128,1>(sXf, dW1, r0d, c0d, fac);
+    {
+      f32x4 bvd = *(const f32x4*)(db1 + c0d);
       f32x4 v;
       #pragma unroll
-      for (int j=0;j<4;j++){ float x = acc[i][j] + bv[j]; v[j] = fmaxf(x, 0.f); }
-      lds4w_f_m8(sY, r0+i, c0, v);
-    }
-  }
-  __syncthreads();
-  if (t < 48){
-    int i = t/3, c = t - i*3;
-    float a = db2[c];
-    for (int k = 0; k < 128; k++) a = fmaf(lds1r_f_m8(sY, i, k), dW2[k*3 + c], a);
-    int n = n0 + i;
-    float f = a / mass[n];
-    float v = vels[n*3 + c] + f;
-    vels[n*3 + c] = v;
-    posw[n*3 + c] += v;
+      for (int jj = 0; jj < 4; jj++){ float x = fac[0][jj] + bvd[jj]; v[jj] = fmaxf(x, 0.f); }
+      lds4w_f_m10(sYf, r0d, c0d, v);
+    }
+    __syncthreads();
+    if (t < 24){
+      int i2 = t/3, c = t - i2*3;
+      float a = db2[c];
+      for (int k = 0; k < H; k++) a = fmaf(lds1r_f_m10(sYf, i2, k), dW2[k*3 + c], a);
+      int n = n0b + i2;
+      float f = a / mass[n];
+      float v = vels[n*3 + c] + f;
+      vels[n*3 + c] = v;
+      posw[n*3 + c] += v;
+    }
   }
 }
 
@@ -724,7 +712,7 @@
 
   auto pack = [&](const float* W, u16* ph, u16* pl, int KS, int L, int lstride, int roff){
     int total = L*8*KS*64;
-    pack_w_m8<<<(total+255)/256, 256, 0, stream>>>(W, ph, pl, KS, L, lstride, roff);
+    pack_w_m10<<<(total+255)/256, 256, 0, stream>>>(W, ph, pl, KS, L, lstride, roff);
   };
   pack(rmW1, p1ah, p1al, 4, NL, 384*H, 0);
   pack(rmW1, p1bh, p1bl, 4, NL, 384*H, 128);
@@ -736,32 +724,32 @@
   pack(omW2, pom2h, pom2l, 4, NL, H*H, 0);
   pack(eW2,  pe2h,  pe2l,  4, 1,  H*H, 0);
 
-  rng_init_m8<<<1, 64, 0, stream>>>(rflags);
-  rng_detect_m8<<<(N_ATOMS*3+255)/256, 256, 0, stream>>>(pos, rflags);
-  rng_select_m8<<<1, 64, 0, stream>>>(rflags, rsel);
-  perturb_m8<<<(N_ATOMS*3+255)/256, 256, 0, stream>>>(pos, rsel, posw, vels);
-  node_enc_m8<<<N_ATOMS, 128, 0, stream>>>(nodef, nW1, nb1, nW2, nb2, xench, xencl);
-  pnode_m8<<<N_ATOMS/16, 256, 0, stream>>>(xench, xencl, p1ah, p1al, p1bh, p1bl, P01g, P02g);
+  rng_init_m10<<<1, 64, 0, stream>>>(rflags);
+  rng_detect_m10<<<(N_ATOMS*3+255)/256, 256, 0, stream>>>(pos, rflags);
+  rng_select_m10<<<1, 64, 0, stream>>>(rflags, rsel);
+  perturb_m10<<<(N_ATOMS*3+255)/256, 256, 0, stream>>>(pos, rsel, posw, vels);
+  node_enc_m10<<<N_ATOMS, 128, 0, stream>>>(nodef, nW1, nb1, nW2, nb2, xench, xencl);
+  pnode_m10<<<N_ATOMS/16, 256, 0, stream>>>(xench, xencl, p1ah, p1al, p1bh, p1bl, P01g, P02g);
 
   for (int s = 0; s < NSTEPS; s++){
     hipMemsetAsync(countsC, 0, (size_t)NCHUNK*N_ATOMS*4, stream);
-    knn_m9<<<N_ATOMS, 256, 0, stream>>>(posw, senders, ea0, countsC);
-    csr_scan2_m9<<<1, 256, 0, stream>>>(countsC, rowstart);
-    csr_place_m9<<<NCHUNK, 1024, 0, stream>>>(senders, countsC, elist);
+    knn_m10<<<N_ATOMS/4, 256, 0, stream>>>(posw, senders, ea0, countsC);
+    csr_scan2_m10<<<1, 256, 0, stream>>>(countsC, rowstart);
+    csr_place_m10<<<NCHUNK, 1024, 0, stream>>>(senders, countsC, elist);
 
     const u16* xch = xench; const u16* xcl = xencl;
     for (int l = 0; l < NL; l++){
       const float* Pa = (l == 0) ? P01g : P1g;
       const float* Pb = (l == 0) ? P02g : P2g;
       if (l == 0){
-        chain_m8<1><<<NE/64, 256, 0, stream>>>(Pa, Pb, eag, senders,
+        chain_m10<1><<<NE/64, 256, 0, stream>>>(Pa, Pb, eag, senders,
             ea0, eW1, eb1, pe2h, pe2l, eb2,
             p1ch  + (size_t)l*S4B, p1cl  + (size_t)l*S4B, rmb1 + l*H,
             prm2h + (size_t)l*S4B, prm2l + (size_t)l*S4B, rmb2 + l*H,
             prm3h + (size_t)l*S4B, prm3l + (size_t)l*S4B, rmb3 + l*H,
             prm4h + (size_t)l*S4B, prm4l + (size_t)l*S4B, rmb4 + l*H);
       } else {
-        chain_m8<0><<<NE/64, 256, 0, stream>>>(Pa, Pb, eag, senders,
+        chain_m10<0><<<NE/64, 256, 0, stream>>>(Pa, Pb, eag, senders,
             ea0, eW1, eb1, pe2h, pe2l, eb2,
             p1ch  + (size_t)l*S4B, p1cl  + (size_t)l*S4B, rmb1 + l*H,
             prm2h + (size_t)l*S4B, prm2l + (size_t)l*S4B, rmb2 + l*H,
@@ -770,16 +758,26 @@
       }
       u16* xnh = (l & 1) ? xAh : xBh;
       u16* xnl = (l & 1) ? xAl : xBl;
-      int lp1 = (l < NL-1) ? (l+1) : l;
-      objagg_m8<<<N_ATOMS/8, 256, 0, stream>>>(xch, xcl, eag, rowstart, elist,
-          pom1h + (size_t)l*S8B, pom1l + (size_t)l*S8B, omb1 + l*H,
-          pom2h + (size_t)l*S4B, pom2l + (size_t)l*S4B, omb2 + l*H,
-          p1ah + (size_t)lp1*S4B, p1al + (size_t)lp1*S4B,
-          p1bh + (size_t)lp1*S4B, p1bl + (size_t)lp1*S4B,
-          xnh, xnl, P1g, P2g);
+      if (l < NL-1){
+        int lp1 = l + 1;
+        objagg_m10<0><<<N_ATOMS/8, 256, 0, stream>>>(xch, xcl, eag, rowstart, elist,
+            pom1h + (size_t)l*S8B, pom1l + (size_t)l*S8B, omb1 + l*H,
+            pom2h + (size_t)l*S4B, pom2l + (size_t)l*S4B, omb2 + l*H,
+            p1ah + (size_t)lp1*S4B, p1al + (size_t)lp1*S4B,
+            p1bh + (size_t)lp1*S4B, p1bl + (size_t)lp1*S4B,
+            xnh, xnl, P1g, P2g,
+            dW1, db1, dW2, db2, mass, posw, vels);
+      } else {
+        objagg_m10<1><<<N_ATOMS/8, 256, 0, stream>>>(xch, xcl, eag, rowstart, elist,
+            pom1h + (size_t)l*S8B, pom1l + (size_t)l*S8B, omb1 + l*H,
+            pom2h + (size_t)l*S4B, pom2l + (size_t)l*S4B, omb2 + l*H,
+            p1ah + (size_t)l*S4B, p1al + (size_t)l*S4B,
+            p1bh + (size_t)l*S4B, p1bl + (size_t)l*S4B,
+            xnh, xnl, P1g, P2g,
+            dW1, db1, dW2, db2, mass, posw, vels);
+      }
       xch = xnh; xcl = xnl;
     }
-    decode_m8<<<N_ATOMS/16, 256, 0, stream>>>(xch, xcl, dW1, db1, dW2, db2, mass, posw, vels);
   }
   hipMemcpyAsync(d_out, posw, (size_t)N_ATOMS*3*4, hipMemcpyDeviceToDevice, stream);
 }
```

Measured after the change: 5.308 ms. 1.03x slower.
